# Kernel tuning notes

Measured on AMD Instinct MI355X. Metric: run time of the kernel, lower is better.

## Reference

```python
import jax, jax.numpy as jnp
import numpy as np

NEG_SLOPE = 0.1


def _conv3d(x, w, b):
    # standard 3x3x3 conv, stride 1, pad 1, NCDHW layout
    y = jax.lax.conv_general_dilated(
        x, w, window_strides=(1, 1, 1), padding=[(1, 1), (1, 1), (1, 1)],
        dimension_numbers=('NCDHW', 'OIDHW', 'NCDHW'))
    return y + b[None, :, None, None, None]


def _deform_conv3d_hw(x, w_off, b_off, w, b):
    """DeformConvPack_d with dimension='HW': 3x3x3 conv whose H/W sampling
    positions are shifted by learned per-location offsets (bilinear sample in
    H,W; integer taps in D). Zero padding outside the volume."""
    B, C, D, H, W = x.shape
    # offset conv: 2 offsets (dh, dw) per kernel tap, 27 taps -> 54 channels
    off = _conv3d(x, w_off, b_off).reshape(B, 27, 2, D, H, W)
    x_flat = x.reshape(B, C, D * H * W)
    d_grid = jnp.arange(D)[:, None, None]          # [D,1,1]
    h_grid = jnp.arange(H)[None, :, None]          # [1,H,1]
    w_grid = jnp.arange(W)[None, None, :]          # [1,1,W]
    out = jnp.zeros((B, w.shape[0], D, H, W), x.dtype)
    k = 0
    for kd in (-1, 0, 1):
        pd = d_grid + kd                            # integer depth tap
        valid_d = (pd >= 0) & (pd < D)
        pdc = jnp.clip(pd, 0, D - 1)
        for kh in (-1, 0, 1):
            for kw in (-1, 0, 1):
                ph = h_grid + kh + off[:, k, 0]     # [B,D,H,W] float
                pw = w_grid + kw + off[:, k, 1]
                h0 = jnp.floor(ph)
                w0 = jnp.floor(pw)
                th = ph - h0                        # bilinear fracs
                tw = pw - w0
                h0i = h0.astype(jnp.int32)
                w0i = w0.astype(jnp.int32)
                samp = jnp.zeros((B, C, D, H, W), x.dtype)
                for dh, wgt_h in ((0, 1.0 - th), (1, th)):
                    hh = h0i + dh
                    vh = (hh >= 0) & (hh < H)
                    hhc = jnp.clip(hh, 0, H - 1)
                    for dw, wgt_w in ((0, 1.0 - tw), (1, tw)):
                        ww = w0i + dw
                        v = valid_d & vh & (ww >= 0) & (ww < W)
                        wwc = jnp.clip(ww, 0, W - 1)
                        idx = (pdc * H + hhc) * W + wwc          # [B,D,H,W]
                        g = jnp.take_along_axis(
                            x_flat, idx.reshape(B, 1, D * H * W), axis=2
                        ).reshape(B, C, D, H, W)
                        wgt = jnp.where(v, wgt_h * wgt_w, 0.0)
                        samp = samp + g * wgt[:, None]
                # accumulate this tap's contribution through the conv weight
                out = out + jnp.einsum('bcdhw,oc->bodhw', samp,
                                       w[:, :, kd + 1, kh + 1, kw + 1])
                k += 1
    return out + b[None, :, None, None, None]


def setup_inputs() -> dict:
    key = jax.random.key(0)
    ks = jax.random.split(key, 9)
    B, nf, D, H, W = 4, 48, 12, 56, 56
    fan = 1.0 / np.sqrt(nf * 27)
    x = jax.random.normal(ks[0], (B, nf, D, H, W), jnp.float32)
    # offset convs: small weights so sampled offsets stay O(1) pixel
    w_off0 = jax.random.normal(ks[1], (54, nf, 3, 3, 3), jnp.float32) * 0.01
    b_off0 = jax.random.normal(ks[2], (54,), jnp.float32) * 0.01
    w0 = jax.random.normal(ks[3], (nf, nf, 3, 3, 3), jnp.float32) * fan
    b0 = jax.random.normal(ks[4], (nf,), jnp.float32) * 0.01
    w_off1 = jax.random.normal(ks[5], (54, nf, 3, 3, 3), jnp.float32) * 0.01
    b_off1 = jax.random.normal(ks[6], (54,), jnp.float32) * 0.01
    w1 = jax.random.normal(ks[7], (nf, nf, 3, 3, 3), jnp.float32) * fan
    b1 = jax.random.normal(ks[8], (nf,), jnp.float32) * 0.01
    return {"x": x, "w_off0": w_off0, "b_off0": b_off0, "w0": w0, "b0": b0,
            "w_off1": w_off1, "b_off1": b_off1, "w1": w1, "b1": b1}


def reference(x, w_off0, b_off0, w0, b0, w_off1, b_off1, w1, b1):
    h = _deform_conv3d_hw(x, w_off0, b_off0, w0, b0)
    h = jnp.where(h >= 0, h, NEG_SLOPE * h)  # LeakyReLU(0.1)
    y = _deform_conv3d_hw(h, w_off1, b_off1, w1, b1)
    return y + x
```

## Files before the change

### kernel.cpp

```cpp
#include <hip/hip_runtime.h>
#include <hip/hip_fp16.h>

constexpr int B_ = 4, C_ = 48, D_ = 12, H_ = 56, W_ = 56;
constexpr int DHW_ = D_ * H_ * W_;
constexpr int NLOC_ = B_ * DHW_;
constexpr int OFFC_ = 54;
constexpr int NXCD_ = 8;

typedef _Float16 f16x8 __attribute__((ext_vector_type(8)));
typedef float f32x4  __attribute__((ext_vector_type(4)));
typedef float f32x2  __attribute__((ext_vector_type(2)));
typedef unsigned int u32x4 __attribute__((ext_vector_type(4)));
typedef unsigned int u32x2 __attribute__((ext_vector_type(2)));

__device__ __forceinline__ int xcd_swizzle(int bid, int nwg) {
    int xcd = bid % NXCD_, lid = bid / NXCD_;
    int q = nwg / NXCD_, r = nwg % NXCD_;
    return (xcd < r ? xcd * (q + 1) : r * (q + 1) + (xcd - r) * q) + lid;
}

__device__ __forceinline__ unsigned short f2h_u(float f) {
    return __builtin_bit_cast(unsigned short, (_Float16)f);
}
__device__ __forceinline__ unsigned int pack_h2(float lo, float hi) {
    return (unsigned int)f2h_u(lo) | ((unsigned int)f2h_u(hi) << 16);
}
__device__ __forceinline__ __half2 bcH(unsigned int u) {
    return __builtin_bit_cast(__half2, u);
}
__device__ __forceinline__ unsigned int bcU(__half2 h) {
    return __builtin_bit_cast(unsigned int, h);
}

__device__ __forceinline__ u32x4 interp4_h(u32x4 c00, u32x4 c01, u32x4 c10, u32x4 c11,
                                           __half2 w0, __half2 w1, __half2 w2, __half2 w3) {
    u32x4 pv;
#pragma unroll
    for (int u = 0; u < 4; ++u) {
        __half2 r = __hmul2(w0, bcH(c00[u]));
        r = __hfma2(w1, bcH(c01[u]), r);
        r = __hfma2(w2, bcH(c10[u]), r);
        r = __hfma2(w3, bcH(c11[u]), r);
        pv[u] = bcU(r);
    }
    return pv;
}

__global__ void __launch_bounds__(256) repack_frag_kernel(
    const float* __restrict__ w, unsigned short* __restrict__ wf, int OC, int MT) {
    int t = blockIdx.x * 256 + threadIdx.x;
    int total = 27 * MT * 1024;
    if (t >= total) return;
    int i    = t & 7;
    int lane = (t >> 3) & 63;
    int ks   = (t >> 9) & 1;
    int mt   = (t >> 10) % MT;
    int k    = t / (MT << 10);
    int oc = mt * 16 + (lane & 15);
    int c  = ks * 32 + 8 * (lane >> 4) + i;
    float v = (oc < OC && c < 48) ? w[((size_t)oc * 48 + c) * 27 + k] : 0.0f;
    wf[t] = f2h_u(v);
}

__global__ void __launch_bounds__(256) to_cl_kernel(const float* __restrict__ x,
                                                    unsigned short* __restrict__ xcl) {
    int loc = blockIdx.x * 256 + threadIdx.x;
    int b = loc / DHW_, s = loc - b * DHW_;
    const float* xp = x + (size_t)b * (C_ * DHW_) + s;
#pragma unroll
    for (int q = 0; q < 6; ++q) {
        float v[8];
#pragma unroll
        for (int u = 0; u < 8; ++u) v[u] = xp[(size_t)(q * 8 + u) * DHW_];
        u32x4 o;
#pragma unroll
        for (int u = 0; u < 4; ++u)
            o[u] = pack_h2(v[2 * u], v[2 * u + 1]);
        *(u32x4*)(xcl + ((size_t)q * NLOC_ + loc) * 8) = o;
    }
}

template <int LEAKY, int RESID, int CLOUT>
__global__ void __launch_bounds__(128) fused_layer(
    const unsigned short* __restrict__ scl,
    const unsigned short* __restrict__ wfo,
    const float* __restrict__ bo,
    const unsigned short* __restrict__ wfc,
    const float* __restrict__ bias,
    const float* __restrict__ resid,
    float* __restrict__ dstf,
    unsigned short* __restrict__ dstcl) {
    __shared__ unsigned short S[2][64][64];
    __shared__ unsigned int OFT[64][29];
    int tid = threadIdx.x, wid = tid >> 6, lane = tid & 63;
    int base = xcd_swizzle(blockIdx.x, gridDim.x) * 64;
    int loc = base + lane;
    int b = loc / DHW_;
    int sp = loc - b * DHW_;
    int w = sp % W_; int t1 = sp / W_;
    int h = t1 % H_; int d = t1 / H_;
    int g = lane >> 4, li = lane & 15, l7 = lane & 7;

    u32x4 z = {0, 0, 0, 0};
    *(u32x4*)&S[wid][lane][(6 ^ l7) * 8] = z;
    *(u32x4*)&S[wid][lane][(7 ^ l7) * 8] = z;

    const u32x4* plane[6];
#pragma unroll
    for (int q = 0; q < 6; ++q)
        plane[q] = (const u32x4*)(scl + ((size_t)q * NLOC_ + (size_t)b * DHW_) * 8);

    {
        f32x4 acc[4][4];
#pragma unroll
        for (int mt = 0; mt < 4; ++mt)
#pragma unroll
            for (int nt = 0; nt < 4; ++nt) acc[mt][nt] = (f32x4){0.f, 0.f, 0.f, 0.f};

#pragma unroll 1
        for (int i = 0; i < 14; ++i) {
            int k = wid + 2 * i;
            if (k >= 27) break;
            int kd = k / 9 - 1, kh = (k / 3) % 3 - 1, kw = k % 3 - 1;
            int pd = d + kd, ph = h + kh, pw = w + kw;
            bool valid = (pd >= 0) & (pd < D_) & (ph >= 0) & (ph < H_) &
                         (pw >= 0) & (pw < W_);
            if (!__any((int)valid)) continue;
            int pdc = min(max(pd, 0), D_ - 1);
            int phc = min(max(ph, 0), H_ - 1);
            int pwc = min(max(pw, 0), W_ - 1);
            int pix = (pdc * H_ + phc) * W_ + pwc;
            u32x4 pv[6];
#pragma unroll
            for (int cc = 0; cc < 6; ++cc) pv[cc] = plane[cc][pix];
#pragma unroll
            for (int cc = 0; cc < 6; ++cc) {
                if (!valid) pv[cc] = z;
                *(u32x4*)&S[wid][lane][(cc ^ l7) * 8] = pv[cc];
            }
            const unsigned short* wk = wfo + (size_t)k * 4096 + lane * 8;
            f16x8 a[4][2];
#pragma unroll
            for (int mt = 0; mt < 4; ++mt)
#pragma unroll
                for (int ks = 0; ks < 2; ++ks)
                    a[mt][ks] = *(const f16x8*)&wk[(mt * 2 + ks) * 512];
#pragma unroll
            for (int nt = 0; nt < 4; ++nt) {
                const unsigned short* sr = &S[wid][nt * 16 + li][0];
                f16x8 b0 = *(const f16x8*)&sr[((0 + g) ^ l7) * 8];
                f16x8 b1 = *(const f16x8*)&sr[((4 + g) ^ l7) * 8];
#pragma unroll
                for (int mt = 0; mt < 4; ++mt) {
                    acc[mt][nt] = __builtin_amdgcn_mfma_f32_16x16x32_f16(a[mt][0], b0, acc[mt][nt], 0, 0, 0);
                    acc[mt][nt] = __builtin_amdgcn_mfma_f32_16x16x32_f16(a[mt][1], b1, acc[mt][nt], 0, 0, 0);
                }
            }
        }

        float* XCH = (float*)&S[0][0][0];
        __syncthreads();
        if (wid == 1) {
#pragma unroll
            for (int mt = 0; mt < 2; ++mt)
#pragma unroll
                for (int nt = 0; nt < 4; ++nt)
                    *(f32x4*)(XCH + (mt * 4 + nt) * 256 + lane * 4) = acc[mt][nt];
        }
        __syncthreads();
        if (wid == 0) {
#pragma unroll
            for (int mt = 0; mt < 2; ++mt)
#pragma unroll
                for (int nt = 0; nt < 4; ++nt)
                    acc[mt][nt] += *(f32x4*)(XCH + (mt * 4 + nt) * 256 + lane * 4);
        }
        __syncthreads();
        if (wid == 1) {
#pragma unroll
            for (int mt = 2; mt < 4; ++mt)
#pragma unroll
                for (int nt = 0; nt < 4; ++nt)
                    *(f32x4*)(XCH + ((mt - 2) * 4 + nt) * 256 + lane * 4) = acc[mt][nt];
        }
        __syncthreads();
        if (wid == 0) {
#pragma unroll
            for (int mt = 2; mt < 4; ++mt)
#pragma unroll
                for (int nt = 0; nt < 4; ++nt)
                    acc[mt][nt] += *(f32x4*)(XCH + ((mt - 2) * 4 + nt) * 256 + lane * 4);
#pragma unroll
            for (int mt = 0; mt < 4; ++mt)
#pragma unroll
                for (int nt = 0; nt < 4; ++nt)
#pragma unroll
                    for (int rp = 0; rp < 2; ++rp) {
                        int oc = mt * 16 + 4 * g + 2 * rp;
                        if (oc < OFFC_) {
                            int kk = mt * 8 + 2 * g + rp;
                            OFT[nt * 16 + li][kk] =
                                pack_h2(acc[mt][nt][2 * rp] + bo[oc],
                                        acc[mt][nt][2 * rp + 1] + bo[oc + 1]);
                        }
                    }
        }
        __syncthreads();
    }

    *(u32x4*)&S[wid][lane][(6 ^ l7) * 8] = z;
    *(u32x4*)&S[wid][lane][(7 ^ l7) * 8] = z;

    f32x4 acc[3][4];
#pragma unroll
    for (int mt = 0; mt < 3; ++mt)
#pragma unroll
        for (int nt = 0; nt < 4; ++nt) acc[mt][nt] = (f32x4){0.f, 0.f, 0.f, 0.f};

#pragma unroll 1
    for (int i = 0; i < 14; ++i) {
        int k = wid + 2 * i;
        if (k >= 27) break;
        int kd = k / 9 - 1, kh = (k / 3) % 3 - 1, kw = k % 3 - 1;
        int pd = d + kd;
        bool vd = (pd >= 0) & (pd < D_);
        if (!__any((int)vd)) continue;
        int pdc = min(max(pd, 0), D_ - 1);

        unsigned int ou = OFT[lane][k];
        __half2 oh2 = bcH(ou);
        float odh = __low2float(oh2), odw = __high2float(oh2);
        float phf = (float)(h + kh) + odh;
        float pwf = (float)(w + kw) + odw;
        float h0f = floorf(phf), w0f = floorf(pwf);
        float th = phf - h0f, tw = pwf - w0f;
        int h0 = (int)h0f, w0 = (int)w0f;

        int pix[4];
        f32x4 cw;
#pragma unroll
        for (int dh = 0; dh < 2; ++dh) {
            int hh = h0 + dh;
            bool vh = vd & (hh >= 0) & (hh < H_);
            int hhc = min(max(hh, 0), H_ - 1);
            float wh = dh ? th : 1.0f - th;
#pragma unroll
            for (int dw = 0; dw < 2; ++dw) {
                int ww = w0 + dw;
                bool v = vh & (ww >= 0) & (ww < W_);
                int wwc = min(max(ww, 0), W_ - 1);
                float wwt = dw ? tw : 1.0f - tw;
                pix[dh * 2 + dw] = (pdc * H_ + hhc) * W_ + wwc;
                cw[dh * 2 + dw] = v ? wh * wwt : 0.0f;
            }
        }
        __half2 w0p = __float2half2_rn(cw[0]);
        __half2 w1p = __float2half2_rn(cw[1]);
        __half2 w2p = __float2half2_rn(cw[2]);
        __half2 w3p = __float2half2_rn(cw[3]);

#pragma unroll
        for (int half = 0; half < 2; ++half) {
            u32x4 st[3][4];
#pragma unroll
            for (int cc = 0; cc < 3; ++cc)
#pragma unroll
                for (int j = 0; j < 4; ++j)
                    st[cc][j] = plane[half * 3 + cc][pix[j]];
#pragma unroll
            for (int cc = 0; cc < 3; ++cc) {
                u32x4 pv = interp4_h(st[cc][0], st[cc][1], st[cc][2], st[cc][3],
                                     w0p, w1p, w2p, w3p);
                *(u32x4*)&S[wid][lane][((half * 3 + cc) ^ l7) * 8] = pv;
            }
        }

        const unsigned short* wk = wfc + (size_t)k * 3072 + lane * 8;
        f16x8 a[3][2];
#pragma unroll
        for (int mt = 0; mt < 3; ++mt)
#pragma unroll
            for (int ks = 0; ks < 2; ++ks)
                a[mt][ks] = *(const f16x8*)&wk[(mt * 2 + ks) * 512];
#pragma unroll
        for (int nt = 0; nt < 4; ++nt) {
            const unsigned short* sr = &S[wid][nt * 16 + li][0];
            f16x8 b0 = *(const f16x8*)&sr[((0 + g) ^ l7) * 8];
            f16x8 b1 = *(const f16x8*)&sr[((4 + g) ^ l7) * 8];
#pragma unroll
            for (int mt = 0; mt < 3; ++mt) {
                acc[mt][nt] = __builtin_amdgcn_mfma_f32_16x16x32_f16(a[mt][0], b0, acc[mt][nt], 0, 0, 0);
                acc[mt][nt] = __builtin_amdgcn_mfma_f32_16x16x32_f16(a[mt][1], b1, acc[mt][nt], 0, 0, 0);
            }
        }
    }

    float* XCH = (float*)&S[1][0][0];
    __syncthreads();
    if (wid == 1) {
#pragma unroll
        for (int mt = 0; mt < 2; ++mt)
#pragma unroll
            for (int nt = 0; nt < 4; ++nt)
                *(f32x4*)(XCH + (mt * 4 + nt) * 256 + lane * 4) = acc[mt][nt];
    }
    __syncthreads();
    if (wid == 0) {
#pragma unroll
        for (int mt = 0; mt < 2; ++mt)
#pragma unroll
            for (int nt = 0; nt < 4; ++nt)
                acc[mt][nt] += *(f32x4*)(XCH + (mt * 4 + nt) * 256 + lane * 4);
    }
    __syncthreads();
    if (wid == 1) {
#pragma unroll
        for (int nt = 0; nt < 4; ++nt)
            *(f32x4*)(XCH + nt * 256 + lane * 4) = acc[2][nt];
    }
    __syncthreads();
    if (wid == 1) return;
#pragma unroll
    for (int nt = 0; nt < 4; ++nt)
        acc[2][nt] += *(f32x4*)(XCH + nt * 256 + lane * 4);

    if (CLOUT) {
        unsigned short* Sb = &S[0][0][0];
#pragma unroll
        for (int mt = 0; mt < 3; ++mt) {
#pragma unroll
            for (int nt = 0; nt < 4; ++nt) {
                float v[4];
#pragma unroll
                for (int r = 0; r < 4; ++r) {
                    int oc = mt * 16 + 4 * g + r;
                    float t = acc[mt][nt][r] + bias[oc];
                    if (LEAKY) t = (t >= 0.f) ? t : 0.1f * t;
                    v[r] = t;
                }
                int row = nt * 16 + li;
                int colb = (mt * 32 + 8 * g) ^ ((li & 7) << 4);
                u32x2 pp = {pack_h2(v[0], v[1]), pack_h2(v[2], v[3])};
                *(u32x2*)((char*)(Sb + (size_t)row * 64) + colb) = pp;
            }
        }
        unsigned short* myrow = Sb + (size_t)lane * 64;
#pragma unroll
        for (int s = 0; s < 6; ++s) {
            u32x4 c = *(u32x4*)((char*)myrow + ((s * 16) ^ ((lane & 7) << 4)));
            *(u32x4*)(dstcl + ((size_t)s * NLOC_ + loc) * 8) = c;
        }
    } else {
        int s0 = base - b * DHW_;
#pragma unroll
        for (int mt = 0; mt < 3; ++mt) {
#pragma unroll
            for (int r = 0; r < 4; ++r) {
                int oc = mt * 16 + 4 * g + r;
                float bb = bias[oc];
#pragma unroll
                for (int nt = 0; nt < 4; ++nt) {
                    size_t addr = ((size_t)b * C_ + oc) * DHW_ + (s0 + nt * 16 + li);
                    float v = acc[mt][nt][r] + bb;
                    if (LEAKY) v = (v >= 0.0f) ? v : 0.1f * v;
                    if (RESID) v += resid[addr];
                    dstf[addr] = v;
                }
            }
        }
    }
}

extern "C" void kernel_launch(void* const* d_in, const int* in_sizes, int n_in,
                              void* d_out, int out_size, void* d_ws, size_t ws_size,
                              hipStream_t stream) {
    const float* x      = (const float*)d_in[0];
    const float* w_off0 = (const float*)d_in[1];
    const float* b_off0 = (const float*)d_in[2];
    const float* w0     = (const float*)d_in[3];
    const float* b0     = (const float*)d_in[4];
    const float* w_off1 = (const float*)d_in[5];
    const float* b_off1 = (const float*)d_in[6];
    const float* w1     = (const float*)d_in[7];
    const float* b1     = (const float*)d_in[8];
    float* out = (float*)d_out;

    unsigned short* xcl = (unsigned short*)d_ws;
    unsigned short* hcl = xcl + (size_t)NLOC_ * 48;
    unsigned short* wf_off  = hcl + (size_t)NLOC_ * 48;
    unsigned short* wf_conv = wf_off + 27 * 4 * 1024;

    dim3 blk128(128), blk256(256);
    int nblk = NLOC_ / 64;

    to_cl_kernel<<<NLOC_ / 256, blk256, 0, stream>>>(x, xcl);

    repack_frag_kernel<<<(27 * 4 * 1024 + 255) / 256, blk256, 0, stream>>>(w_off0, wf_off, OFFC_, 4);
    repack_frag_kernel<<<(27 * 3 * 1024 + 255) / 256, blk256, 0, stream>>>(w0, wf_conv, C_, 3);
    fused_layer<1, 0, 1><<<nblk, blk128, 0, stream>>>(xcl, wf_off, b_off0, wf_conv, b0,
                                                      nullptr, nullptr, hcl);

    repack_frag_kernel<<<(27 * 4 * 1024 + 255) / 256, blk256, 0, stream>>>(w_off1, wf_off, OFFC_, 4);
    repack_frag_kernel<<<(27 * 3 * 1024 + 255) / 256, blk256, 0, stream>>>(w1, wf_conv, C_, 3);
    fused_layer<0, 1, 0><<<nblk, blk128, 0, stream>>>(hcl, wf_off, b_off1, wf_conv, b1,
                                                      x, out, nullptr);
}
```

Baseline: 259.1 us.

## Split offset-conv MFMA work by output channels instead of kernel taps across waves

The offset convolution previously split the 27 taps between the two waves, each computing all 64 output-channel rows, then reduced partial sums through shared memory with four barriers. Now each wave loops over all 27 taps but computes only its half of the output-channel tiles and writes its offsets directly, with no cross-wave reduction. This drops the LDS exchange, several barriers and half the accumulator registers. In exchange each wave gathers the full set of input pixels for every tap, doubling gather loads and LDS staging per wave, and the zeroing of the padding slots between stages is removed.

```diff
diff --git a/kernel.cpp b/kernel.cpp
--- a/kernel.cpp
+++ b/kernel.cpp
@@ -9,7 +9,6 @@
 
 typedef _Float16 f16x8 __attribute__((ext_vector_type(8)));
 typedef float f32x4  __attribute__((ext_vector_type(4)));
-typedef float f32x2  __attribute__((ext_vector_type(2)));
 typedef unsigned int u32x4 __attribute__((ext_vector_type(4)));
 typedef unsigned int u32x2 __attribute__((ext_vector_type(2)));
 
@@ -111,16 +110,14 @@
         plane[q] = (const u32x4*)(scl + ((size_t)q * NLOC_ + (size_t)b * DHW_) * 8);
 
     {
-        f32x4 acc[4][4];
-#pragma unroll
-        for (int mt = 0; mt < 4; ++mt)
-#pragma unroll
-            for (int nt = 0; nt < 4; ++nt) acc[mt][nt] = (f32x4){0.f, 0.f, 0.f, 0.f};
+        f32x4 acc[2][4];
+#pragma unroll
+        for (int m = 0; m < 2; ++m)
+#pragma unroll
+            for (int nt = 0; nt < 4; ++nt) acc[m][nt] = (f32x4){0.f, 0.f, 0.f, 0.f};
 
 #pragma unroll 1
-        for (int i = 0; i < 14; ++i) {
-            int k = wid + 2 * i;
-            if (k >= 27) break;
+        for (int k = 0; k < 27; ++k) {
             int kd = k / 9 - 1, kh = (k / 3) % 3 - 1, kw = k % 3 - 1;
             int pd = d + kd, ph = h + kh, pw = w + kw;
             bool valid = (pd >= 0) & (pd < D_) & (ph >= 0) & (ph < H_) &
@@ -139,77 +136,43 @@
                 *(u32x4*)&S[wid][lane][(cc ^ l7) * 8] = pv[cc];
             }
             const unsigned short* wk = wfo + (size_t)k * 4096 + lane * 8;
-            f16x8 a[4][2];
-#pragma unroll
-            for (int mt = 0; mt < 4; ++mt)
+            f16x8 a[2][2];
+#pragma unroll
+            for (int m = 0; m < 2; ++m)
 #pragma unroll
                 for (int ks = 0; ks < 2; ++ks)
-                    a[mt][ks] = *(const f16x8*)&wk[(mt * 2 + ks) * 512];
+                    a[m][ks] = *(const f16x8*)&wk[((2 * wid + m) * 2 + ks) * 512];
 #pragma unroll
             for (int nt = 0; nt < 4; ++nt) {
                 const unsigned short* sr = &S[wid][nt * 16 + li][0];
                 f16x8 b0 = *(const f16x8*)&sr[((0 + g) ^ l7) * 8];
                 f16x8 b1 = *(const f16x8*)&sr[((4 + g) ^ l7) * 8];
 #pragma unroll
-                for (int mt = 0; mt < 4; ++mt) {
-                    acc[mt][nt] = __builtin_amdgcn_mfma_f32_16x16x32_f16(a[mt][0], b0, acc[mt][nt], 0, 0, 0);
-                    acc[mt][nt] = __builtin_amdgcn_mfma_f32_16x16x32_f16(a[mt][1], b1, acc[mt][nt], 0, 0, 0);
+                for (int m = 0; m < 2; ++m) {
+                    acc[m][nt] = __builtin_amdgcn_mfma_f32_16x16x32_f16(a[m][0], b0, acc[m][nt], 0, 0, 0);
+                    acc[m][nt] = __builtin_amdgcn_mfma_f32_16x16x32_f16(a[m][1], b1, acc[m][nt], 0, 0, 0);
                 }
             }
         }
 
-        float* XCH = (float*)&S[0][0][0];
+#pragma unroll
+        for (int m = 0; m < 2; ++m) {
+            int mt = 2 * wid + m;
+#pragma unroll
+            for (int nt = 0; nt < 4; ++nt)
+#pragma unroll
+                for (int rp = 0; rp < 2; ++rp) {
+                    int oc = mt * 16 + 4 * g + 2 * rp;
+                    if (oc < OFFC_) {
+                        int kk = mt * 8 + 2 * g + rp;
+                        OFT[nt * 16 + li][kk] =
+                            pack_h2(acc[m][nt][2 * rp] + bo[oc],
+                                    acc[m][nt][2 * rp + 1] + bo[oc + 1]);
+                    }
+                }
+        }
         __syncthreads();
-        if (wid == 1) {
-#pragma unroll
-            for (int mt = 0; mt < 2; ++mt)
-#pragma unroll
-                for (int nt = 0; nt < 4; ++nt)
-                    *(f32x4*)(XCH + (mt * 4 + nt) * 256 + lane * 4) = acc[mt][nt];
-        }
-        __syncthreads();
-        if (wid == 0) {
-#pragma unroll
-            for (int mt = 0; mt < 2; ++mt)
-#pragma unroll
-                for (int nt = 0; nt < 4; ++nt)
-                    acc[mt][nt] += *(f32x4*)(XCH + (mt * 4 + nt) * 256 + lane * 4);
-        }
-        __syncthreads();
-        if (wid == 1) {
-#pragma unroll
-            for (int mt = 2; mt < 4; ++mt)
-#pragma unroll
-                for (int nt = 0; nt < 4; ++nt)
-                    *(f32x4*)(XCH + ((mt - 2) * 4 + nt) * 256 + lane * 4) = acc[mt][nt];
-        }
-        __syncthreads();
-        if (wid == 0) {
-#pragma unroll
-            for (int mt = 2; mt < 4; ++mt)
-#pragma unroll
-                for (int nt = 0; nt < 4; ++nt)
-                    acc[mt][nt] += *(f32x4*)(XCH + ((mt - 2) * 4 + nt) * 256 + lane * 4);
-#pragma unroll
-            for (int mt = 0; mt < 4; ++mt)
-#pragma unroll
-                for (int nt = 0; nt < 4; ++nt)
-#pragma unroll
-                    for (int rp = 0; rp < 2; ++rp) {
-                        int oc = mt * 16 + 4 * g + 2 * rp;
-                        if (oc < OFFC_) {
-                            int kk = mt * 8 + 2 * g + rp;
-                            OFT[nt * 16 + li][kk] =
-                                pack_h2(acc[mt][nt][2 * rp] + bo[oc],
-                                        acc[mt][nt][2 * rp + 1] + bo[oc + 1]);
-                        }
-                    }
-        }
-        __syncthreads();
-    }
-
-    *(u32x4*)&S[wid][lane][(6 ^ l7) * 8] = z;
-    *(u32x4*)&S[wid][lane][(7 ^ l7) * 8] = z;
+    }
 
     f32x4 acc[3][4];
 #pragma unroll
```

New measurement: 271.5 us. 4.8% more time.
